# Performance work log

Measured on AMD Instinct MI355X. Metric: run time of the kernel, lower is better.

The kernel has to match this reference:

```python
import jax, jax.numpy as jnp
import numpy as np

B, C, N, K_CAND, K_TOP = 8, 16, 65536, 10, 4

def setup_inputs() -> dict:
    key = jax.random.key(0)
    k1, k2, k3, k4, k5, k6 = jax.random.split(key, 6)
    scale = 1.0 / np.sqrt(2 * C)  # conv2d default init scale for fan_in=32
    return {
        "original_features": jax.random.normal(k1, (B, C, N), dtype=jnp.float32),
        "sampled_features": jax.random.normal(k2, (B, C, N, K_CAND), dtype=jnp.float32),
        "w1": jax.random.uniform(k3, (2 * C,), jnp.float32, -scale, scale),
        "b1": jax.random.uniform(k4, (), jnp.float32, -scale, scale),
        "w2": jax.random.uniform(k5, (2 * C,), jnp.float32, -scale, scale),
        "b2": jax.random.uniform(k6, (), jnp.float32, -scale, scale),
    }

def reference(original_features, sampled_features, w1, b1, w2, b2):
    # original_features: [B,C,N]; sampled_features: [B,C,N,K_CAND]
    # 1x1 conv over concat([repeated_orig, sampled]) == two channel contractions
    wo1, ws1 = w1[:C], w1[C:]
    # similarity scores: [B,N,K_CAND]
    sim = jax.nn.sigmoid(
        jnp.einsum('bcn,c->bn', original_features, wo1)[:, :, None]
        + jnp.einsum('bcnk,c->bnk', sampled_features, ws1)
        + b1)
    _, topk_idx = jax.lax.top_k(sim, K_TOP)  # [B,N,K_TOP]
    idx = jnp.broadcast_to(topk_idx[:, None, :, :], (sim.shape[0], C, sim.shape[1], K_TOP))
    topk_features = jnp.take_along_axis(sampled_features, idx, axis=-1)  # [B,C,N,K_TOP]
    wo2, ws2 = w2[:C], w2[C:]
    recal = jax.nn.sigmoid(
        jnp.einsum('bcn,c->bn', original_features, wo2)[:, :, None]
        + jnp.einsum('bcnk,c->bnk', topk_features, ws2)
        + b2)  # [B,N,K_TOP]
    summed = jnp.einsum('bcnk,bnk->bcn', topk_features, recal)
    return original_features + summed
```

## Files before the change

kernel.cpp:

```cpp
#include <hip/hip_runtime.h>
#include <math.h>

#define BB 8
#define CC 16
#define NN 65536
#define KC 10
#define KT 4

#define PTW 8
#define BLK 128
#define PTB 16
#define WFLT (PTW * CC * KC)

typedef __attribute__((address_space(3))) void lds_t;
typedef __attribute__((address_space(1))) void glob_t;

__global__ __launch_bounds__(BLK, 8) void swg_kernel(
    const float* __restrict__ orig,
    const float* __restrict__ samp,
    const float* __restrict__ w1,
    const float* __restrict__ w2,
    const float* __restrict__ b2p,
    float* __restrict__ out)
{
    __shared__ float buf[2 * WFLT];

    const int t   = threadIdx.x;
    const int l   = t & 63;
    const int w   = t >> 6;
    const int bid = blockIdx.x;

    const int b   = bid >> 12;
    const int n0w = ((bid * PTB) & (NN - 1)) + w * PTW;

    const float4* sampB4 = (const float4*)samp
        + (size_t)b * ((size_t)CC * NN * KC / 4);
    const int n0q = n0w * (KC / 2) / 2;

    float* ldsw = buf + w * WFLT;

#pragma unroll
    for (int j = 0; j < 5; ++j) {
        const int m = j * 64 + l;
        const int c = m / 20;
        const int r = m - c * 20;
        __builtin_amdgcn_global_load_lds(
            (const glob_t*)(sampB4 + (size_t)c * (NN * KC / 4) + n0q + r),
            (lds_t*)((char*)ldsw + j * 1024), 16, 0, 0);
    }

    const int q = l & 7;
    const int p = l >> 3;
    const int n = n0w + p;

    float o[2];
#pragma unroll
    for (int cc = 0; cc < 2; ++cc)
        o[cc] = orig[(size_t)(b * CC + q + 8 * cc) * NN + n];

    float ws1[2], wo2[2], ws2[2];
#pragma unroll
    for (int cc = 0; cc < 2; ++cc) {
        const int c = q + 8 * cc;
        ws1[cc] = w1[CC + c];
        wo2[cc] = w2[c];
        ws2[cc] = w2[CC + c];
    }
    const float b2 = b2p[0];

    asm volatile("s_waitcnt vmcnt(0)" ::: "memory");

    float v[2][KC];
#pragma unroll
    for (int cc = 0; cc < 2; ++cc) {
        const float* base = ldsw + (q + 8 * cc) * (PTW * KC) + p * KC;
#pragma unroll
        for (int j = 0; j < 5; ++j) {
            const float2 x = *(const float2*)(base + 2 * j);
            v[cc][2 * j]     = x.x;
            v[cc][2 * j + 1] = x.y;
        }
    }

    float s[KC];
    float dO = o[0] * wo2[0] + o[1] * wo2[1];
#pragma unroll
    for (int k = 0; k < KC; ++k)
        s[k] = v[0][k] * ws1[0] + v[1][k] * ws1[1];
#pragma unroll
    for (int m = 1; m <= 4; m <<= 1) {
        dO += __shfl_xor(dO, m, 64);
#pragma unroll
        for (int k = 0; k < KC; ++k) s[k] += __shfl_xor(s[k], m, 64);
    }

    unsigned selmask = 0;
#pragma unroll
    for (int k = 0; k < KC; ++k) {
        int rk = 0;
#pragma unroll
        for (int j = 0; j < KC; ++j) {
            if (j == k) continue;
            const bool beats = (j < k) ? (s[j] >= s[k]) : (s[j] > s[k]);
            rk += beats ? 1 : 0;
        }
        selmask |= (rk < KT) ? (1u << k) : 0u;
    }

    float d2[KC];
#pragma unroll
    for (int k = 0; k < KC; ++k)
        d2[k] = v[0][k] * ws2[0] + v[1][k] * ws2[1];
#pragma unroll
    for (int m = 1; m <= 4; m <<= 1) {
#pragma unroll
        for (int k = 0; k < KC; ++k) d2[k] += __shfl_xor(d2[k], m, 64);
    }

    float sum0 = 0.f, sum1 = 0.f;
#pragma unroll
    for (int k = 0; k < KC; ++k) {
        const float x   = dO + d2[k] + b2;
        const float sig = __builtin_amdgcn_rcpf(1.f + __expf(-x));
        const float wk  = ((selmask >> k) & 1u) ? sig : 0.f;
        sum0 += v[0][k] * wk;
        sum1 += v[1][k] * wk;
    }
    out[(size_t)(b * CC + q)     * NN + n] = o[0] + sum0;
    out[(size_t)(b * CC + q + 8) * NN + n] = o[1] + sum1;
}

extern "C" void kernel_launch(void* const* d_in, const int* in_sizes, int n_in,
                              void* d_out, int out_size, void* d_ws, size_t ws_size,
                              hipStream_t stream) {
    const float* orig = (const float*)d_in[0];
    const float* samp = (const float*)d_in[1];
    const float* w1   = (const float*)d_in[2];
    const float* w2   = (const float*)d_in[4];
    const float* b2   = (const float*)d_in[5];
    float* out = (float*)d_out;

    const int grid = (BB * NN) / PTB;
    hipLaunchKernelGGL(swg_kernel, dim3(grid), dim3(BLK), 0, stream,
                       orig, samp, w1, w2, b2, out);
}
```

Before: 88.33 us.

## Use 32-point blocks with register-staged LDS loads and coalesced orig staging

Each block now covers 32 points with 256 threads instead of two independent 8-point waves. Sampled features are copied into shared memory through ordinary float4 global loads and LDS stores, replacing the direct global-to-LDS path, and a block-wide barrier synchronises the tile. Original features are read as coalesced float4 rows into a padded LDS buffer rather than as scattered scalar loads. Per-row contiguous runs get longer and orig access is better coalesced, at the cost of a __syncthreads, extra register traffic and slightly lower occupancy bounds.

```diff
diff --git a/kernel.cpp b/kernel.cpp
--- a/kernel.cpp
+++ b/kernel.cpp
@@ -7,15 +7,10 @@
 #define KC 10
 #define KT 4
 
-#define PTW 8
-#define BLK 128
-#define PTB 16
-#define WFLT (PTW * CC * KC)
+#define TPTS 32
+#define BLK  256
 
-typedef __attribute__((address_space(3))) void lds_t;
-typedef __attribute__((address_space(1))) void glob_t;
-
-__global__ __launch_bounds__(BLK, 8) void swg_kernel(
+__global__ __launch_bounds__(BLK, 7) void swg_kernel(
     const float* __restrict__ orig,
     const float* __restrict__ samp,
     const float* __restrict__ w1,
@@ -23,57 +18,51 @@
     const float* __restrict__ b2p,
     float* __restrict__ out)
 {
-    __shared__ float buf[2 * WFLT];
+    __shared__ float4 s4[CC * TPTS * KC / 4];
+    __shared__ float  obuf[CC * 33];
 
     const int t   = threadIdx.x;
-    const int l   = t & 63;
-    const int w   = t >> 6;
     const int bid = blockIdx.x;
+    const int b   = bid >> 11;
+    const int n0  = (bid & 2047) * TPTS;
 
-    const int b   = bid >> 12;
-    const int n0w = ((bid * PTB) & (NN - 1)) + w * PTW;
+    {
+        const int sc = t >> 4;
+        const int sl = t & 15;
+        const float4* g4 = (const float4*)(samp + ((size_t)(b * CC + sc) * NN + n0) * KC);
+        float4* l4 = s4 + sc * (TPTS * KC / 4);
+#pragma unroll
+        for (int j = 0; j < 5; ++j)
+            l4[j * 16 + sl] = g4[j * 16 + sl];
+    }
+    if (t < 128) {
+        const int oc = t >> 3;
+        const int ol = t & 7;
+        const float4 x = *(const float4*)(orig + (size_t)(b * CC + oc) * NN + n0 + ol * 4);
+        float* dst = obuf + oc * 33 + ol * 4;
+        dst[0] = x.x; dst[1] = x.y; dst[2] = x.z; dst[3] = x.w;
+    }
+    __syncthreads();
 
-    const float4* sampB4 = (const float4*)samp
-        + (size_t)b * ((size_t)CC * NN * KC / 4);
-    const int n0q = n0w * (KC / 2) / 2;
+    const int q = t & 7;
+    const int p = t >> 3;
+    const int n = n0 + p;
 
-    float* ldsw = buf + w * WFLT;
-
-#pragma unroll
-    for (int j = 0; j < 5; ++j) {
-        const int m = j * 64 + l;
-        const int c = m / 20;
-        const int r = m - c * 20;
-        __builtin_amdgcn_global_load_lds(
-            (const glob_t*)(sampB4 + (size_t)c * (NN * KC / 4) + n0q + r),
-            (lds_t*)((char*)ldsw + j * 1024), 16, 0, 0);
-    }
-
-    const int q = l & 7;
-    const int p = l >> 3;
-    const int n = n0w + p;
-
-    float o[2];
-#pragma unroll
-    for (int cc = 0; cc < 2; ++cc)
-        o[cc] = orig[(size_t)(b * CC + q + 8 * cc) * NN + n];
-
-    float ws1[2], wo2[2], ws2[2];
+    const float b2 = b2p[0];
+    float ws1[2], wo2[2], ws2[2], o[2];
 #pragma unroll
     for (int cc = 0; cc < 2; ++cc) {
         const int c = q + 8 * cc;
         ws1[cc] = w1[CC + c];
         wo2[cc] = w2[c];
         ws2[cc] = w2[CC + c];
+        o[cc]   = obuf[c * 33 + p];
     }
-    const float b2 = b2p[0];
-
-    asm volatile("s_waitcnt vmcnt(0)" ::: "memory");
 
     float v[2][KC];
 #pragma unroll
     for (int cc = 0; cc < 2; ++cc) {
-        const float* base = ldsw + (q + 8 * cc) * (PTW * KC) + p * KC;
+        const float* base = (const float*)s4 + (q + 8 * cc) * (TPTS * KC) + p * KC;
 #pragma unroll
         for (int j = 0; j < 5; ++j) {
             const float2 x = *(const float2*)(base + 2 * j);
@@ -140,7 +129,7 @@
     const float* b2   = (const float*)d_in[5];
     float* out = (float*)d_out;
 
-    const int grid = (BB * NN) / PTB;
+    const int grid = (BB * NN) / TPTS;
     hipLaunchKernelGGL(swg_kernel, dim3(grid), dim3(BLK), 0, stream,
                        orig, samp, w1, w2, b2, out);
 }
```

Result: slower. 97.68 us (+10.6%).
